# Kernel optimization log

Hardware: AMD Instinct MI355X
Metric: run time of the kernel (lower is better)

## Reference

```python
import jax, jax.numpy as jnp
import numpy as np
from jax import lax

SPAN = 11
K = 2 * SPAN + 1          # 23 -> 529 offsets
SIG_RGB = 0.1
SIG_XY = 6.0
LAM = 0.15
B, C, H, W = 2, 3, 160, 160


def _patches(x):
    """x: (N, C, H, W) -> (N, C, K, K, H, W), zero-padded.
    patch[di, dj] at pixel (i, j) equals x[i + di - SPAN, j + dj - SPAN],
    matching the torch module's shifted-slice double loop (dx = di - SPAN)."""
    n, c, h, w = x.shape
    xp = jnp.pad(x, ((0, 0), (0, 0), (SPAN, SPAN), (SPAN, SPAN)))

    def get(off):
        di = off // K
        dj = off % K
        return lax.dynamic_slice(xp, (0, 0, di, dj), (n, c, h, w))

    p = jax.vmap(get)(jnp.arange(K * K))              # (K*K, N, C, H, W)
    return p.reshape(K, K, n, c, h, w).transpose(2, 3, 0, 1, 4, 5)


def setup_inputs() -> dict:
    key = jax.random.key(0)
    k1, k2, k3, k4, k5 = jax.random.split(key, 5)
    logit = jax.random.normal(k1, (B, C, H, W), jnp.float32)
    target = jax.random.randint(k2, (B, H, W), 0, C)
    # small-magnitude image so exp(-0.5*(x - patch/0.1)^2) does not fully underflow
    image = jax.random.uniform(k3, (B, 3, H, W), jnp.float32) * 0.1
    source_map = (jax.random.uniform(k4, (B, 1, H, W)) > 0.5).astype(jnp.float32)
    destination_map = (jax.random.uniform(k5, (B, H, W)) > 0.5).astype(jnp.float32)
    return dict(logit=logit, target=target, image=image,
                source_map=source_map, destination_map=destination_map)


def _gcrf(image, y_hat, source_map, m_dst):
    b, c, h, w = y_hat.shape
    img_p = _patches(image)                                  # (B,3,K,K,H,W)
    valid = _patches(jnp.ones((1, 1, h, w), image.dtype))[0, 0]  # (K,K,H,W) in-bounds mask
    # NOTE: faithful to source bug: only the shifted feature is divided by sigma
    drgb = image[:, :, None, None] - img_p / SIG_RGB
    k_rgb = jnp.exp(-0.5 * jnp.sum(drgb * drgb, axis=1))     # (B,K,K,H,W)
    ii, jj = jnp.meshgrid(jnp.arange(h, dtype=image.dtype),
                          jnp.arange(w, dtype=image.dtype), indexing='ij')
    idx = jnp.stack([ii, jj])[None]                          # (1,2,H,W)
    idx_p = _patches(idx)[0]                                 # (2,K,K,H,W)
    dxy = idx[0][:, None, None] - idx_p / SIG_XY
    k_xy = jnp.exp(-0.5 * jnp.sum(dxy * dxy, axis=0))        # (K,K,H,W)
    kmat = (k_rgb + k_xy[None]) * valid[None]                # out-of-bounds offsets stay 0
    m_src = _patches(source_map)[:, 0]                       # (B,K,K,H,W)
    Kg = kmat * m_src * m_dst[:, None, None]                 # gated kernel
    U = _patches(y_hat)                                      # (B,C,K,K,H,W)
    Egy = jnp.einsum('bcijhw,bijhw->bchw', U, Kg)            # sum over window
    temp = jnp.einsum('bchw,bdhw->bcd', Egy, y_hat)          # (B,C,C)
    Moff = 1.0 - jnp.eye(c, dtype=y_hat.dtype)               # off-diagonal compatibility
    return jnp.sum(Moff * temp) / (b * h * w)


def reference(logit, target, image, source_map, destination_map):
    y_hat = jax.nn.softmax(logit, axis=1)
    m_dst = 1.0 - destination_map
    L_gcrf = _gcrf(image, y_hat, source_map, m_dst)
    logp = jax.nn.log_softmax(logit, axis=1)
    L_ce = -jnp.take_along_axis(logp, target[:, None], axis=1)[:, 0]  # (B,H,W)
    L_ce = jnp.mean(L_ce * destination_map)
    return L_ce + LAM * L_gcrf
```

## Files before the change

### kernel.cpp

```cpp
#include <hip/hip_runtime.h>

#define Bn 2
#define Cn 3
#define Hn 160
#define Wn 160
#define SPANc 11
#define Kc 23
#define HWn (Hn * Wn)
#define PW 182
#define PP (PW * PW)
#define LAMc 0.15f
#define TJ 32
#define Gc 4
#define TI 32
#define NROW (TI + Kc - 1)
#define NREC (NROW * TJ)
#define CEXP (-0.72134752f)
#define SRGB_S (0.84932190f)
#define NPREP ((Bn * PP + 255) / 256)

__device__ __forceinline__ float wave_reduce64(float v) {
#pragma unroll
    for (int off = 32; off > 0; off >>= 1) v += __shfl_down(v, off, 64);
    return v;
}

__device__ __forceinline__ unsigned int bf16pk(float a, float b) {
    unsigned int ua = __float_as_uint(a), ub = __float_as_uint(b);
    ua += 0x7fffu + ((ua >> 16) & 1u);
    ub += 0x7fffu + ((ub >> 16) & 1u);
    return (ua & 0xffff0000u) | (ub >> 16);
}

__global__ __launch_bounds__(256) void prep_kernel(
    const float* __restrict__ logit, const int* __restrict__ target,
    const float* __restrict__ image, const float* __restrict__ srcmap,
    const float* __restrict__ dstmap, uint2* __restrict__ gU2,
    unsigned int* __restrict__ gU1, float4* __restrict__ cvec,
    float* __restrict__ pc, double* __restrict__ acc)
{
    int idx = blockIdx.x * 256 + threadIdx.x;
    float ce = 0.0f;
    if (idx < Bn * PP) {
        int b   = idx / PP;
        int rem = idx - b * PP;
        int ip  = rem / PW;
        int jp  = rem - ip * PW;
        int i = ip - SPANc, j = jp - SPANc;
        if ((unsigned)i < (unsigned)Hn && (unsigned)j < (unsigned)Wn) {
            int r = i * Wn + j;
            int p = b * HWn + r;
            const float* lg = logit + (size_t)b * Cn * HWn + r;
            float l0 = lg[0], l1 = lg[HWn], l2 = lg[2 * HWn];
            float m = fmaxf(l0, fmaxf(l1, l2));
            float e0 = __expf(l0 - m), e1 = __expf(l1 - m), e2 = __expf(l2 - m);
            float s = e0 + e1 + e2;
            float inv = 1.0f / s;
            float y0 = e0 * inv, y1 = e1 * inv, y2 = e2 * inv;
            float lse = m + __logf(s);

            const float* im = image + (size_t)b * 3 * HWn + r;
            float i0v = im[0] * SRGB_S, i1v = im[HWn] * SRGB_S, i2v = im[2 * HWn] * SRGB_S;
            float sv = srcmap[p];
            float dv = dstmap[p];

            gU2[idx] = make_uint2(bf16pk(i0v, i1v), bf16pk(i2v, sv * y0));
            gU1[idx] = bf16pk(sv * y1, sv * y2);

            float md = LAMc * (1.0f - dv);
            cvec[p] = make_float4(md * (1.0f - y0), md * (1.0f - y1),
                                  md * (1.0f - y2), 0.0f);

            int t = target[p];
            float lt = (t == 0) ? l0 : ((t == 1) ? l1 : l2);
            ce = (lse - lt) * dv;
        } else {
            gU2[idx] = make_uint2(0u, 0u);
            gU1[idx] = 0u;
        }
    }
    if (idx == 0) *acc = 0.0;

    float v = wave_reduce64(ce);
    __shared__ float wsum[4];
    int tid = threadIdx.x;
    if ((tid & 63) == 0) wsum[tid >> 6] = v;
    __syncthreads();
    if (tid == 0) pc[blockIdx.x] = wsum[0] + wsum[1] + wsum[2] + wsum[3];
}

template<bool XY>
__device__ __forceinline__ void tap(float p0, float p1, float p2,
                                    float q0, float q1, float q2,
                                    float cA0, float cA1, float cA2,
                                    bool xy_on, float dy2, float dxv,
                                    float& e0, float& e1, float& e2)
{
    float d0 = fmaf(p0, -10.0f, cA0);
    float d1 = fmaf(p1, -10.0f, cA1);
    float d2 = fmaf(p2, -10.0f, cA2);
    float ss = fmaf(d0, d0, fmaf(d1, d1, d2 * d2));
    float k = exp2f(-ss);
    if constexpr (XY) {
        if (xy_on) k += exp2f(fmaf(dxv, dxv, dy2) * CEXP);
    }
    e0 = fmaf(k, q0, e0);
    e1 = fmaf(k, q1, e1);
    e2 = fmaf(k, q2, e2);
}

template<bool XY>
__device__ __forceinline__ void window_loop(
    const uint2* sU2, const unsigned int* sU1, int lbase,
    const float* cA0, const float* cA1, const float* cA2,
    bool xy_on, float dy2, float fi0, float eg[Gc][3])
{
#pragma unroll
    for (int r = 0; r < 3; ++r) {
        uint2 ru = sU2[lbase + r * TJ];
        unsigned int rv = sU1[lbase + r * TJ];
        float p0 = __uint_as_float(ru.x & 0xffff0000u);
        float p1 = __uint_as_float(ru.x << 16);
        float p2 = __uint_as_float(ru.y & 0xffff0000u);
        float q0 = __uint_as_float(ru.y << 16);
        float q1 = __uint_as_float(rv & 0xffff0000u);
        float q2 = __uint_as_float(rv << 16);
        float dxb = XY ? (fi0 - (fi0 + (float)(r - SPANc)) * (1.0f / 6.0f)) : 0.0f;
#pragma unroll
        for (int c = 0; c < 3; ++c) {
            if (c > r) continue;
            tap<XY>(p0, p1, p2, q0, q1, q2, cA0[c], cA1[c], cA2[c], xy_on, dy2,
                    dxb + (float)c, eg[c][0], eg[c][1], eg[c][2]);
        }
    }
#pragma unroll 2
    for (int r = 3; r <= 22; ++r) {
        uint2 ru = sU2[lbase + r * TJ];
        unsigned int rv = sU1[lbase + r * TJ];
        float p0 = __uint_as_float(ru.x & 0xffff0000u);
        float p1 = __uint_as_float(ru.x << 16);
        float p2 = __uint_as_float(ru.y & 0xffff0000u);
        float q0 = __uint_as_float(ru.y << 16);
        float q1 = __uint_as_float(rv & 0xffff0000u);
        float q2 = __uint_as_float(rv << 16);
        float dxb = XY ? (fi0 - (fi0 + (float)(r - SPANc)) * (1.0f / 6.0f)) : 0.0f;
#pragma unroll
        for (int c = 0; c < Gc; ++c) {
            tap<XY>(p0, p1, p2, q0, q1, q2, cA0[c], cA1[c], cA2[c], xy_on, dy2,
                    dxb + (float)c, eg[c][0], eg[c][1], eg[c][2]);
        }
    }
#pragma unroll
    for (int r = 23; r <= 25; ++r) {
        uint2 ru = sU2[lbase + r * TJ];
        unsigned int rv = sU1[lbase + r * TJ];
        float p0 = __uint_as_float(ru.x & 0xffff0000u);
        float p1 = __uint_as_float(ru.x << 16);
        float p2 = __uint_as_float(ru.y & 0xffff0000u);
        float q0 = __uint_as_float(ru.y << 16);
        float q1 = __uint_as_float(rv & 0xffff0000u);
        float q2 = __uint_as_float(rv << 16);
        float dxb = XY ? (fi0 - (fi0 + (float)(r - SPANc)) * (1.0f / 6.0f)) : 0.0f;
#pragma unroll
        for (int c = 1; c < Gc; ++c) {
            if (c < r - 22) continue;
            tap<XY>(p0, p1, p2, q0, q1, q2, cA0[c], cA1[c], cA2[c], xy_on, dy2,
                    dxb + (float)c, eg[c][0], eg[c][1], eg[c][2]);
        }
    }
}

__global__ __launch_bounds__(256, 4) void gcrf_kernel(
    const uint2* __restrict__ gU2, const unsigned int* __restrict__ gU1,
    const float4* __restrict__ cvec, double* __restrict__ acc)
{
    __shared__ uint2 sU2[NREC];
    __shared__ unsigned int sU1[NREC];

    int tx = threadIdx.x;
    int ty = threadIdx.y;
    int tid = ty * TJ + tx;
    int jx = blockIdx.x;
    int j  = jx * TJ + tx;
    int by = blockIdx.y;
    int b  = by / 5;
    int it = by - b * 5;
    int i0g = it * TI + ty * Gc;
    int dj = blockIdx.z;

    size_t g0 = (size_t)b * PP + (size_t)(it * TI) * PW + (jx * TJ + dj);
    for (int n = tid; n < NREC; n += 256) {
        int rr = n >> 5, cc = n & 31;
        size_t gi = g0 + (size_t)rr * PW + cc;
        sU2[n] = gU2[gi];
        sU1[n] = gU1[gi];
    }
    __syncthreads();

    int lbase = ty * Gc * TJ + tx;
    float cA0[Gc], cA1[Gc], cA2[Gc];
#pragma unroll
    for (int c = 0; c < Gc; ++c) {
        uint2 cu = sU2[lbase + (c + SPANc) * TJ];
        cA0[c] = __uint_as_float(cu.x & 0xffff0000u);
        cA1[c] = __uint_as_float(cu.x << 16);
        cA2[c] = __uint_as_float(cu.y & 0xffff0000u);
    }

    bool xy_on = (j < 16) && (i0g < 16);
    float dy = (float)j - (float)(j + dj - SPANc) * (1.0f / 6.0f);
    float dy2 = dy * dy;
    float fi0 = (float)i0g;

    float eg[Gc][3];
#pragma unroll
    for (int c = 0; c < Gc; ++c) { eg[c][0] = 0.f; eg[c][1] = 0.f; eg[c][2] = 0.f; }

    if (jx == 0 && it == 0) {
        window_loop<true>(sU2, sU1, lbase, cA0, cA1, cA2, xy_on, dy2, fi0, eg);
    } else {
        window_loop<false>(sU2, sU1, lbase, cA0, cA1, cA2, false, dy2, fi0, eg);
    }

    const float4* cv = cvec + ((size_t)b * HWn + (size_t)i0g * Wn + j);
    float contrib = 0.0f;
#pragma unroll
    for (int c = 0; c < Gc; ++c) {
        float4 t = cv[(size_t)c * Wn];
        contrib += eg[c][0] * t.x + eg[c][1] * t.y + eg[c][2] * t.z;
    }

    float v = wave_reduce64(contrib);
    __shared__ float wsum[4];
    if ((tid & 63) == 0) wsum[tid >> 6] = v;
    __syncthreads();
    if (tid == 0) atomicAdd(acc, (double)(wsum[0] + wsum[1] + wsum[2] + wsum[3]));
}

__global__ __launch_bounds__(256) void finalize_kernel(
    const float* __restrict__ pc, const double* __restrict__ acc,
    float* __restrict__ out)
{
    int t = threadIdx.x;
    float s = 0.0f;
    if (t < NPREP) s += pc[t];
    if (t + 256 < NPREP) s += pc[t + 256];
    float v = wave_reduce64(s);
    __shared__ float wsum[4];
    if ((t & 63) == 0) wsum[t >> 6] = v;
    __syncthreads();
    if (t == 0) {
        double tot = acc[0] + (double)(wsum[0] + wsum[1] + wsum[2] + wsum[3]);
        out[0] = (float)(tot * (1.0 / (double)(Bn * HWn)));
    }
}

extern "C" void kernel_launch(void* const* d_in, const int* in_sizes, int n_in,
                              void* d_out, int out_size, void* d_ws, size_t ws_size,
                              hipStream_t stream)
{
    const float* logit  = (const float*)d_in[0];
    const int*   target = (const int*)d_in[1];
    const float* image  = (const float*)d_in[2];
    const float* srcmap = (const float*)d_in[3];
    const float* dstmap = (const float*)d_in[4];
    float* out = (float*)d_out;

    const size_t NRECG = (size_t)Bn * PP;
    double*       acc  = (double*)d_ws;
    float*        pc   = (float*)((char*)d_ws + 256);
    uint2*        gU2  = (uint2*)((char*)d_ws + 4096);
    unsigned int* gU1  = (unsigned int*)((char*)d_ws + 4096 + NRECG * 8);
    float4*       cvec = (float4*)((char*)d_ws + 4096 + NRECG * 12);

    prep_kernel<<<NPREP, 256, 0, stream>>>(logit, target, image, srcmap, dstmap,
                                           gU2, gU1, cvec, pc, acc);
    dim3 grid(Wn / TJ, (Hn / TI) * Bn, Kc);
    dim3 blk(TJ, 8);
    gcrf_kernel<<<grid, blk, 0, stream>>>(gU2, gU1, cvec, acc);
    finalize_kernel<<<1, 256, 0, stream>>>(pc, acc, out);
}
```

Before: 86.00 us.

## Expand RGB Gaussian exponent into dot product and fold finalize into main kernel

Rewrites the per-tap RGB distance as a precomputed linear form. A per-neighbour constant (-B) is packed alongside the features, and the center terms are prescaled, so each tap costs three FMAs plus an exp instead of subtract-square-accumulate. Packs all features into one 16-byte uint4 record instead of separate uint2/uint1 arrays. It also removes the finalize kernel by having one gcrf block add the CE partial sums, using float atomics on the output with prescaled terms. The trade-offs are larger shared memory per record, a possible loss of precision from bf16 storage of the expanded B term, and non-double float atomics.

```diff
diff --git a/kernel.cpp b/kernel.cpp
--- a/kernel.cpp
+++ b/kernel.cpp
@@ -10,13 +10,15 @@
 #define PW 182
 #define PP (PW * PW)
 #define LAMc 0.15f
+#define INVN (1.0f / (float)(Bn * HWn))
 #define TJ 32
 #define Gc 4
 #define TI 32
 #define NROW (TI + Kc - 1)
 #define NREC (NROW * TJ)
 #define CEXP (-0.72134752f)
-#define SRGB_S (0.84932190f)
+#define CX   (14.42695041f)
+#define CA   (0.72134752f)
 #define NPREP ((Bn * PP + 255) / 256)
 
 __device__ __forceinline__ float wave_reduce64(float v) {
@@ -35,9 +37,8 @@
 __global__ __launch_bounds__(256) void prep_kernel(
     const float* __restrict__ logit, const int* __restrict__ target,
     const float* __restrict__ image, const float* __restrict__ srcmap,
-    const float* __restrict__ dstmap, uint2* __restrict__ gU2,
-    unsigned int* __restrict__ gU1, float4* __restrict__ cvec,
-    float* __restrict__ pc, double* __restrict__ acc)
+    const float* __restrict__ dstmap, uint4* __restrict__ gU4,
+    float4* __restrict__ cvec, float* __restrict__ pc, float* __restrict__ out)
 {
     int idx = blockIdx.x * 256 + threadIdx.x;
     float ce = 0.0f;
@@ -60,26 +61,26 @@
             float lse = m + __logf(s);
 
             const float* im = image + (size_t)b * 3 * HWn + r;
-            float i0v = im[0] * SRGB_S, i1v = im[HWn] * SRGB_S, i2v = im[2 * HWn] * SRGB_S;
+            float p0 = im[0], p1 = im[HWn], p2 = im[2 * HWn];
             float sv = srcmap[p];
             float dv = dstmap[p];
 
-            gU2[idx] = make_uint2(bf16pk(i0v, i1v), bf16pk(i2v, sv * y0));
-            gU1[idx] = bf16pk(sv * y1, sv * y2);
-
-            float md = LAMc * (1.0f - dv);
+            float B = (p0 * p0 + p1 * p1 + p2 * p2) * (100.0f * CA);
+            gU4[idx] = make_uint4(bf16pk(p0, p1), bf16pk(p2, -B),
+                                  bf16pk(sv * y0, sv * y1), bf16pk(sv * y2, 0.0f));
+
+            float md = LAMc * (1.0f - dv) * INVN;
             cvec[p] = make_float4(md * (1.0f - y0), md * (1.0f - y1),
                                   md * (1.0f - y2), 0.0f);
 
             int t = target[p];
             float lt = (t == 0) ? l0 : ((t == 1) ? l1 : l2);
-            ce = (lse - lt) * dv;
+            ce = (lse - lt) * dv * INVN;
         } else {
-            gU2[idx] = make_uint2(0u, 0u);
-            gU1[idx] = 0u;
-        }
-    }
-    if (idx == 0) *acc = 0.0;
+            gU4[idx] = make_uint4(0u, 0u, 0u, 0u);
+        }
+    }
+    if (idx == 0) out[0] = 0.0f;
 
     float v = wave_reduce64(ce);
     __shared__ float wsum[4];
@@ -90,17 +91,14 @@
 }
 
 template<bool XY>
-__device__ __forceinline__ void tap(float p0, float p1, float p2,
+__device__ __forceinline__ void tap(float p0, float p1, float p2, float mB,
                                     float q0, float q1, float q2,
-                                    float cA0, float cA1, float cA2,
+                                    float c0s, float c1s, float c2s, float mA,
                                     bool xy_on, float dy2, float dxv,
                                     float& e0, float& e1, float& e2)
 {
-    float d0 = fmaf(p0, -10.0f, cA0);
-    float d1 = fmaf(p1, -10.0f, cA1);
-    float d2 = fmaf(p2, -10.0f, cA2);
-    float ss = fmaf(d0, d0, fmaf(d1, d1, d2 * d2));
-    float k = exp2f(-ss);
+    float e = fmaf(c0s, p0, fmaf(c1s, p1, fmaf(c2s, p2, mB)));
+    float k = exp2f(e + mA);
     if constexpr (XY) {
         if (xy_on) k += exp2f(fmaf(dxv, dxv, dy2) * CEXP);
     }
@@ -111,71 +109,70 @@
 
 template<bool XY>
 __device__ __forceinline__ void window_loop(
-    const uint2* sU2, const unsigned int* sU1, int lbase,
-    const float* cA0, const float* cA1, const float* cA2,
+    const uint4* sU4, int lbase,
+    const float* c0s, const float* c1s, const float* c2s, const float* mA,
     bool xy_on, float dy2, float fi0, float eg[Gc][3])
 {
 #pragma unroll
     for (int r = 0; r < 3; ++r) {
-        uint2 ru = sU2[lbase + r * TJ];
-        unsigned int rv = sU1[lbase + r * TJ];
+        uint4 ru = sU4[lbase + r * TJ];
         float p0 = __uint_as_float(ru.x & 0xffff0000u);
         float p1 = __uint_as_float(ru.x << 16);
         float p2 = __uint_as_float(ru.y & 0xffff0000u);
-        float q0 = __uint_as_float(ru.y << 16);
-        float q1 = __uint_as_float(rv & 0xffff0000u);
-        float q2 = __uint_as_float(rv << 16);
+        float mB = __uint_as_float(ru.y << 16);
+        float q0 = __uint_as_float(ru.z & 0xffff0000u);
+        float q1 = __uint_as_float(ru.z << 16);
+        float q2 = __uint_as_float(ru.w & 0xffff0000u);
         float dxb = XY ? (fi0 - (fi0 + (float)(r - SPANc)) * (1.0f / 6.0f)) : 0.0f;
 #pragma unroll
         for (int c = 0; c < 3; ++c) {
             if (c > r) continue;
-            tap<XY>(p0, p1, p2, q0, q1, q2, cA0[c], cA1[c], cA2[c], xy_on, dy2,
-                    dxb + (float)c, eg[c][0], eg[c][1], eg[c][2]);
+            tap<XY>(p0, p1, p2, mB, q0, q1, q2, c0s[c], c1s[c], c2s[c], mA[c],
+                    xy_on, dy2, dxb + (float)c, eg[c][0], eg[c][1], eg[c][2]);
         }
     }
 #pragma unroll 2
     for (int r = 3; r <= 22; ++r) {
-        uint2 ru = sU2[lbase + r * TJ];
-        unsigned int rv = sU1[lbase + r * TJ];
+        uint4 ru = sU4[lbase + r * TJ];
         float p0 = __uint_as_float(ru.x & 0xffff0000u);
         float p1 = __uint_as_float(ru.x << 16);
         float p2 = __uint_as_float(ru.y & 0xffff0000u);
-        float q0 = __uint_as_float(ru.y << 16);
-        float q1 = __uint_as_float(rv & 0xffff0000u);
-        float q2 = __uint_as_float(rv << 16);
+        float mB = __uint_as_float(ru.y << 16);
+        float q0 = __uint_as_float(ru.z & 0xffff0000u);
+        float q1 = __uint_as_float(ru.z << 16);
+        float q2 = __uint_as_float(ru.w & 0xffff0000u);
         float dxb = XY ? (fi0 - (fi0 + (float)(r - SPANc)) * (1.0f / 6.0f)) : 0.0f;
 #pragma unroll
         for (int c = 0; c < Gc; ++c) {
-            tap<XY>(p0, p1, p2, q0, q1, q2, cA0[c], cA1[c], cA2[c], xy_on, dy2,
-                    dxb + (float)c, eg[c][0], eg[c][1], eg[c][2]);
+            tap<XY>(p0, p1, p2, mB, q0, q1, q2, c0s[c], c1s[c], c2s[c], mA[c],
+                    xy_on, dy2, dxb + (float)c, eg[c][0], eg[c][1], eg[c][2]);
         }
     }
 #pragma unroll
     for (int r = 23; r <= 25; ++r) {
-        uint2 ru = sU2[lbase + r * TJ];
-        unsigned int rv = sU1[lbase + r * TJ];
+        uint4 ru = sU4[lbase + r * TJ];
         float p0 = __uint_as_float(ru.x & 0xffff0000u);
         float p1 = __uint_as_float(ru.x << 16);
         float p2 = __uint_as_float(ru.y & 0xffff0000u);
-        float q0 = __uint_as_float(ru.y << 16);
-        float q1 = __uint_as_float(rv & 0xffff0000u);
-        float q2 = __uint_as_float(rv << 16);
+        float mB = __uint_as_float(ru.y << 16);
+        float q0 = __uint_as_float(ru.z & 0xffff0000u);
+        float q1 = __uint_as_float(ru.z << 16);
+        float q2 = __uint_as_float(ru.w & 0xffff0000u);
         float dxb = XY ? (fi0 - (fi0 + (float)(r - SPANc)) * (1.0f / 6.0f)) : 0.0f;
 #pragma unroll
         for (int c = 1; c < Gc; ++c) {
             if (c < r - 22) continue;
-            tap<XY>(p0, p1, p2, q0, q1, q2, cA0[c], cA1[c], cA2[c], xy_on, dy2,
-                    dxb + (float)c, eg[c][0], eg[c][1], eg[c][2]);
+            tap<XY>(p0, p1, p2, mB, q0, q1, q2, c0s[c], c1s[c], c2s[c], mA[c],
+                    xy_on, dy2, dxb + (float)c, eg[c][0], eg[c][1], eg[c][2]);
         }
     }
 }
 
 __global__ __launch_bounds__(256, 4) void gcrf_kernel(
-    const uint2* __restrict__ gU2, const unsigned int* __restrict__ gU1,
-    const float4* __restrict__ cvec, double* __restrict__ acc)
-{
-    __shared__ uint2 sU2[NREC];
-    __shared__ unsigned int sU1[NREC];
+    const uint4* __restrict__ gU4, const float4* __restrict__ cvec,
+    const float* __restrict__ pc, float* __restrict__ out)
+{
+    __shared__ uint4 sU4[NREC];
 
     int tx = threadIdx.x;
     int ty = threadIdx.y;
@@ -191,20 +188,20 @@
     size_t g0 = (size_t)b * PP + (size_t)(it * TI) * PW + (jx * TJ + dj);
     for (int n = tid; n < NREC; n += 256) {
         int rr = n >> 5, cc = n & 31;
-        size_t gi = g0 + (size_t)rr * PW + cc;
-        sU2[n] = gU2[gi];
-        sU1[n] = gU1[gi];
+        sU4[n] = gU4[g0 + (size_t)rr * PW + cc];
     }
     __syncthreads();
 
     int lbase = ty * Gc * TJ + tx;
-    float cA0[Gc], cA1[Gc], cA2[Gc];
+    float c0s[Gc], c1s[Gc], c2s[Gc], mA[Gc];
 #pragma unroll
     for (int c = 0; c < Gc; ++c) {
-        uint2 cu = sU2[lbase + (c + SPANc) * TJ];
-        cA0[c] = __uint_as_float(cu.x & 0xffff0000u);
-        cA1[c] = __uint_as_float(cu.x << 16);
-        cA2[c] = __uint_as_float(cu.y & 0xffff0000u);
+        uint4 cu = sU4[lbase + (c + SPANc) * TJ];
+        float cc0 = __uint_as_float(cu.x & 0xffff0000u);
+        float cc1 = __uint_as_float(cu.x << 16);
+        float cc2 = __uint_as_float(cu.y & 0xffff0000u);
+        c0s[c] = cc0 * CX; c1s[c] = cc1 * CX; c2s[c] = cc2 * CX;
+        mA[c] = -CA * fmaf(cc0, cc0, fmaf(cc1, cc1, cc2 * cc2));
     }
 
     bool xy_on = (j < 16) && (i0g < 16);
@@ -217,9 +214,9 @@
     for (int c = 0; c < Gc; ++c) { eg[c][0] = 0.f; eg[c][1] = 0.f; eg[c][2] = 0.f; }
 
     if (jx == 0 && it == 0) {
-        window_loop<true>(sU2, sU1, lbase, cA0, cA1, cA2, xy_on, dy2, fi0, eg);
+        window_loop<true>(sU4, lbase, c0s, c1s, c2s, mA, xy_on, dy2, fi0, eg);
     } else {
-        window_loop<false>(sU2, sU1, lbase, cA0, cA1, cA2, false, dy2, fi0, eg);
+        window_loop<false>(sU4, lbase, c0s, c1s, c2s, mA, false, dy2, fi0, eg);
     }
 
     const float4* cv = cvec + ((size_t)b * HWn + (size_t)i0g * Wn + j);
@@ -234,24 +231,17 @@
     __shared__ float wsum[4];
     if ((tid & 63) == 0) wsum[tid >> 6] = v;
     __syncthreads();
-    if (tid == 0) atomicAdd(acc, (double)(wsum[0] + wsum[1] + wsum[2] + wsum[3]));
-}
-
-__global__ __launch_bounds__(256) void finalize_kernel(
-    const float* __restrict__ pc, const double* __restrict__ acc,
-    float* __restrict__ out)
-{
-    int t = threadIdx.x;
-    float s = 0.0f;
-    if (t < NPREP) s += pc[t];
-    if (t + 256 < NPREP) s += pc[t + 256];
-    float v = wave_reduce64(s);
-    __shared__ float wsum[4];
-    if ((t & 63) == 0) wsum[t >> 6] = v;
-    __syncthreads();
-    if (t == 0) {
-        double tot = acc[0] + (double)(wsum[0] + wsum[1] + wsum[2] + wsum[3]);
-        out[0] = (float)(tot * (1.0 / (double)(Bn * HWn)));
+    if (tid == 0) atomicAdd(out, wsum[0] + wsum[1] + wsum[2] + wsum[3]);
+
+    if (jx == 4 && by == 9 && dj == 22) {
+        float s = 0.0f;
+        if (tid < NPREP) s += pc[tid];
+        if (tid + 256 < NPREP) s += pc[tid + 256];
+        float v2 = wave_reduce64(s);
+        __syncthreads();
+        if ((tid & 63) == 0) wsum[tid >> 6] = v2;
+        __syncthreads();
+        if (tid == 0) atomicAdd(out, wsum[0] + wsum[1] + wsum[2] + wsum[3]);
     }
 }
 
@@ -267,16 +257,13 @@
     float* out = (float*)d_out;
 
     const size_t NRECG = (size_t)Bn * PP;
-    double*       acc  = (double*)d_ws;
-    float*        pc   = (float*)((char*)d_ws + 256);
-    uint2*        gU2  = (uint2*)((char*)d_ws + 4096);
-    unsigned int* gU1  = (unsigned int*)((char*)d_ws + 4096 + NRECG * 8);
-    float4*       cvec = (float4*)((char*)d_ws + 4096 + NRECG * 12);
+    float*  pc   = (float*)((char*)d_ws + 256);
+    uint4*  gU4  = (uint4*)((char*)d_ws + 4096);
+    float4* cvec = (float4*)((char*)d_ws + 4096 + NRECG * 16);
 
     prep_kernel<<<NPREP, 256, 0, stream>>>(logit, target, image, srcmap, dstmap,
-                                           gU2, gU1, cvec, pc, acc);
+                                           gU4, cvec, pc, out);
     dim3 grid(Wn / TJ, (Hn / TI) * Bn, Kc);
     dim3 blk(TJ, 8);
-    gcrf_kernel<<<grid, blk, 0, stream>>>(gU2, gU1, cvec, acc);
-    finalize_kernel<<<1, 256, 0, stream>>>(pc, acc, out);
-}
+    gcrf_kernel<<<grid, blk, 0, stream>>>(gU4, cvec, pc, out);
+}
```

New measurement: 85.23 us. About the same (-0.9%).
